# Kernel tuning notes

Measured on AMD Instinct MI355X. Metric: run time of the kernel, lower is better.

Reference implementation:

```python
import jax, jax.numpy as jnp
import numpy as np

B, N, DIM, H, DH = 4, 1024, 1024, 16, 64
SCALE = DH ** -0.5

def setup_inputs() -> dict:
    key = jax.random.key(0)
    ks = jax.random.split(key, 6)
    s = DIM ** -0.5
    return {
        "x": jax.random.normal(ks[0], (B, N, DIM), jnp.float32),
        "Wq": jax.random.normal(ks[1], (DIM, H * DH), jnp.float32) * s,
        "Wk": jax.random.normal(ks[2], (DIM, H * DH), jnp.float32) * s,
        "Wv": jax.random.normal(ks[3], (DIM, H * DH), jnp.float32) * s,
        "Wo": jax.random.normal(ks[4], (H * DH, DIM), jnp.float32) * s,
        "bo": jnp.zeros((DIM,), jnp.float32),
    }

def reference(x, Wq, Wk, Wv, Wo, bo):
    # context is None -> context = x (self-attention), no mask
    split = lambda t: t.reshape(B, N, H, DH).transpose(0, 2, 1, 3)  # b n (h d) -> b h n d
    q = split(x @ Wq)
    k = split(x @ Wk)
    v = split(x @ Wv)
    dots = jnp.einsum('bhid,bhjd->bhij', q, k) * SCALE
    attn = jax.nn.softmax(dots, axis=-1)
    out = jnp.einsum('bhij,bhjd->bhid', attn, v)
    out = out.transpose(0, 2, 1, 3).reshape(B, N, H * DH)  # b h n d -> b n (h d)
    out = out @ Wo + bo  # dropout p=0.0 is identity
    return (out, attn)
```

## Files before the change

### kernel.cpp

```cpp
#include <hip/hip_runtime.h>


#define NN   1024
#define HH   16
#define DHD  64
#define HDD  1024
#define SCALE_ 0.125f

typedef unsigned short ushort_t;
typedef __attribute__((ext_vector_type(8))) short short8;
typedef __attribute__((ext_vector_type(4))) float f32x4;

__device__ __forceinline__ ushort_t f2bf(float f) {
    unsigned int u = __float_as_uint(f);
    u += 0x7fffu + ((u >> 16) & 1u);
    return (ushort_t)(u >> 16);
}

__global__ void transposeW(const float* __restrict__ src, ushort_t* __restrict__ dst) {
    __shared__ ushort_t t[32][33];
    const int bx = blockIdx.x * 32, by = blockIdx.y * 32;
    const int x = threadIdx.x;
#pragma unroll
    for (int yo = 0; yo < 32; yo += 8) {
        int y = threadIdx.y + yo;
        t[y][x] = f2bf(src[(size_t)(by + y) * 1024 + bx + x]);
    }
    __syncthreads();
#pragma unroll
    for (int yo = 0; yo < 32; yo += 8) {
        int y = threadIdx.y + yo;
        dst[(size_t)(bx + y) * 1024 + by + x] = t[x][y];
    }
}

__global__ __launch_bounds__(256)
void gemm_qkv(const float* __restrict__ A,
              const ushort_t* __restrict__ BT0, const ushort_t* __restrict__ BT1,
              const ushort_t* __restrict__ BT2,
              ushort_t* __restrict__ C0, ushort_t* __restrict__ C1,
              ushort_t* __restrict__ C2) {
    __shared__ __align__(16) ushort_t As[128][72];
    __shared__ __align__(16) ushort_t Bs[128][72];

    const int z = blockIdx.z;
    const ushort_t* BT = (z == 0) ? BT0 : (z == 1) ? BT1 : BT2;
    ushort_t* C = (z == 0) ? C0 : (z == 1) ? C1 : C2;
    const int vt_mode = (z == 2) ? 1 : 0;

    const int tid = threadIdx.x;
    const int wave = tid >> 6, lane = tid & 63;
    const int quad = lane >> 4, lr = lane & 15;
    const int wr = (wave >> 1) << 6;
    const int wc = (wave & 1) << 6;
    const int m0 = blockIdx.y << 7;
    const int n0 = blockIdx.x << 7;

    f32x4 acc[4][4];
#pragma unroll
    for (int i = 0; i < 4; i++)
#pragma unroll
        for (int j = 0; j < 4; j++) acc[i][j] = (f32x4){0.f, 0.f, 0.f, 0.f};

    for (int k0 = 0; k0 < 1024; k0 += 64) {
        __syncthreads();
#pragma unroll
        for (int it = 0; it < 4; it++) {
            int idx = tid + it * 256;
            int row = idx >> 3, ch = (idx & 7) << 3;
            const float* ap = A + (size_t)(m0 + row) * 1024 + k0 + ch;
            float4 f0 = *(const float4*)ap;
            float4 f1 = *(const float4*)(ap + 4);
            ushort_t* d = &As[row][ch];
            d[0] = f2bf(f0.x); d[1] = f2bf(f0.y); d[2] = f2bf(f0.z); d[3] = f2bf(f0.w);
            d[4] = f2bf(f1.x); d[5] = f2bf(f1.y); d[6] = f2bf(f1.z); d[7] = f2bf(f1.w);
            *(uint4*)&Bs[row][ch] = *(const uint4*)(BT + (size_t)(n0 + row) * 1024 + k0 + ch);
        }
        __syncthreads();
#pragma unroll
        for (int kk = 0; kk < 64; kk += 32) {
            short8 a[4], b[4];
#pragma unroll
            for (int i = 0; i < 4; i++)
                a[i] = *(const short8*)&As[wr + i * 16 + lr][kk + quad * 8];
#pragma unroll
            for (int j = 0; j < 4; j++)
                b[j] = *(const short8*)&Bs[wc + j * 16 + lr][kk + quad * 8];
#pragma unroll
            for (int i = 0; i < 4; i++)
#pragma unroll
                for (int j = 0; j < 4; j++)
                    acc[i][j] = __builtin_amdgcn_mfma_f32_16x16x32_bf16(
                        a[i], b[j], acc[i][j], 0, 0, 0);
        }
    }

    if (vt_mode == 0) {
#pragma unroll
        for (int i = 0; i < 4; i++)
#pragma unroll
            for (int j = 0; j < 4; j++) {
                int col = n0 + wc + j * 16 + lr;
                int rowb = m0 + wr + i * 16 + quad * 4;
#pragma unroll
                for (int ii = 0; ii < 4; ii++)
                    C[(size_t)(rowb + ii) * 1024 + col] = f2bf(acc[i][j][ii]);
            }
    } else {
#pragma unroll
        for (int i = 0; i < 4; i++)
#pragma unroll
            for (int j = 0; j < 4; j++) {
                int c = n0 + wc + j * 16 + lr;
                int h = c >> 6, d = c & 63;
                int rowb = m0 + wr + i * 16 + quad * 4;
#pragma unroll
                for (int ii = 0; ii < 4; ii++) {
                    int m = rowb + ii;
                    int b_ = m >> 10, n_ = m & 1023;
                    C[((size_t)((b_ * HH + h) * DHD + d) << 10) + n_] = f2bf(acc[i][j][ii]);
                }
            }
    }
}

__global__ __launch_bounds__(256)
void gemm_out(const ushort_t* __restrict__ A, const ushort_t* __restrict__ BT,
              const float* __restrict__ bias, float* __restrict__ C) {
    __shared__ __align__(16) ushort_t As[128][72];
    __shared__ __align__(16) ushort_t Bs[128][72];

    const int tid = threadIdx.x;
    const int wave = tid >> 6, lane = tid & 63;
    const int quad = lane >> 4, lr = lane & 15;
    const int wr = (wave >> 1) << 6;
    const int wc = (wave & 1) << 6;
    const int m0 = blockIdx.y << 7;
    const int n0 = blockIdx.x << 7;

    f32x4 acc[4][4];
#pragma unroll
    for (int i = 0; i < 4; i++)
#pragma unroll
        for (int j = 0; j < 4; j++) acc[i][j] = (f32x4){0.f, 0.f, 0.f, 0.f};

    for (int k0 = 0; k0 < 1024; k0 += 64) {
        __syncthreads();
#pragma unroll
        for (int it = 0; it < 4; it++) {
            int idx = tid + it * 256;
            int row = idx >> 3, ch = (idx & 7) << 3;
            *(uint4*)&As[row][ch] = *(const uint4*)(A + (size_t)(m0 + row) * 1024 + k0 + ch);
            *(uint4*)&Bs[row][ch] = *(const uint4*)(BT + (size_t)(n0 + row) * 1024 + k0 + ch);
        }
        __syncthreads();
#pragma unroll
        for (int kk = 0; kk < 64; kk += 32) {
            short8 a[4], b[4];
#pragma unroll
            for (int i = 0; i < 4; i++)
                a[i] = *(const short8*)&As[wr + i * 16 + lr][kk + quad * 8];
#pragma unroll
            for (int j = 0; j < 4; j++)
                b[j] = *(const short8*)&Bs[wc + j * 16 + lr][kk + quad * 8];
#pragma unroll
            for (int i = 0; i < 4; i++)
#pragma unroll
                for (int j = 0; j < 4; j++)
                    acc[i][j] = __builtin_amdgcn_mfma_f32_16x16x32_bf16(
                        a[i], b[j], acc[i][j], 0, 0, 0);
        }
    }

#pragma unroll
    for (int i = 0; i < 4; i++)
#pragma unroll
        for (int j = 0; j < 4; j++) {
            int col = n0 + wc + j * 16 + lr;
            float badd = bias[col];
            int rowb = m0 + wr + i * 16 + quad * 4;
#pragma unroll
            for (int ii = 0; ii < 4; ii++)
                C[(size_t)(rowb + ii) * 1024 + col] = acc[i][j][ii] + badd;
        }
}

__global__ __launch_bounds__(256)
void attn_kernel(const ushort_t* __restrict__ Q, const ushort_t* __restrict__ K,
                 const ushort_t* __restrict__ VT, float* __restrict__ attn,
                 ushort_t* __restrict__ O) {
    __shared__ __align__(16) ushort_t Qs[64][72];
    __shared__ __align__(16) ushort_t Ks[128][72];
    __shared__ __align__(16) ushort_t Vs[64][136];
    __shared__ __align__(16) ushort_t Ps[64][136];

    const int tid = threadIdx.x;
    const int wave = tid >> 6, lane = tid & 63;
    const int quad = lane >> 4, lr = lane & 15;
    const int q0 = blockIdx.x << 6;
    const int h = blockIdx.y;
    const int b = blockIdx.z;

    const ushort_t* Qb = Q + (size_t)b * NN * HDD + h * DHD;
    const ushort_t* Kb = K + (size_t)b * NN * HDD + h * DHD;
    const ushort_t* VTb = VT + (size_t)(b * HH + h) * DHD * NN;
    float* attn_b = attn + (size_t)(b * HH + h) * NN * NN;
    ushort_t* Ob = O + (size_t)b * NN * HDD + h * DHD;

#pragma unroll
    for (int it = 0; it < 2; it++) {
        int idx = tid + it * 256;
        int row = idx >> 3, ch = (idx & 7) << 3;
        *(uint4*)&Qs[row][ch] = *(const uint4*)(Qb + (size_t)(q0 + row) * HDD + ch);
    }
    __syncthreads();
    const short8 aq0 = *(const short8*)&Qs[wave * 16 + lr][quad * 8];
    const short8 aq1 = *(const short8*)&Qs[wave * 16 + lr][32 + quad * 8];

    float m_i[4], l_i[4];
#pragma unroll
    for (int ii = 0; ii < 4; ii++) { m_i[ii] = -1e30f; l_i[ii] = 0.f; }

    for (int kb = 0; kb < 8; kb++) {
        __syncthreads();
#pragma unroll
        for (int it = 0; it < 4; it++) {
            int idx = tid + it * 256;
            int row = idx >> 3, ch = (idx & 7) << 3;
            *(uint4*)&Ks[row][ch] =
                *(const uint4*)(Kb + (size_t)(kb * 128 + row) * HDD + ch);
        }
        __syncthreads();
        f32x4 s[8];
#pragma unroll
        for (int cb = 0; cb < 8; cb++) {
            s[cb] = (f32x4){0.f, 0.f, 0.f, 0.f};
            short8 b0 = *(const short8*)&Ks[cb * 16 + lr][quad * 8];
            short8 b1 = *(const short8*)&Ks[cb * 16 + lr][32 + quad * 8];
            s[cb] = __builtin_amdgcn_mfma_f32_16x16x32_bf16(aq0, b0, s[cb], 0, 0, 0);
            s[cb] = __builtin_amdgcn_mfma_f32_16x16x32_bf16(aq1, b1, s[cb], 0, 0, 0);
        }
#pragma unroll
        for (int ii = 0; ii < 4; ii++) {
            float rmax = -1e30f;
#pragma unroll
            for (int cb = 0; cb < 8; cb++) rmax = fmaxf(rmax, s[cb][ii]);
            rmax *= SCALE_;
#pragma unroll
            for (int off = 1; off < 16; off <<= 1)
                rmax = fmaxf(rmax, __shfl_xor(rmax, off));
            float mnew = fmaxf(m_i[ii], rmax);
            float psum = 0.f;
#pragma unroll
            for (int cb = 0; cb < 8; cb++) psum += __expf(s[cb][ii] * SCALE_ - mnew);
#pragma unroll
            for (int off = 1; off < 16; off <<= 1) psum += __shfl_xor(psum, off);
            l_i[ii] = l_i[ii] * __expf(m_i[ii] - mnew) + psum;
            m_i[ii] = mnew;
        }
    }
    float inv_l[4];
#pragma unroll
    for (int ii = 0; ii < 4; ii++) inv_l[ii] = 1.f / l_i[ii];

    f32x4 oacc[4];
#pragma unroll
    for (int db = 0; db < 4; db++) oacc[db] = (f32x4){0.f, 0.f, 0.f, 0.f};

    for (int kb = 0; kb < 8; kb++) {
        __syncthreads();
#pragma unroll
        for (int it = 0; it < 8; it++) {
            int idx = tid + it * 256;
            if (idx < 1024) {
                int row = idx >> 3, ch = (idx & 7) << 3;
                *(uint4*)&Ks[row][ch] =
                    *(const uint4*)(Kb + (size_t)(kb * 128 + row) * HDD + ch);
            } else {
                int j = idx - 1024;
                int row = j >> 4, ch = (j & 15) << 3;
                *(uint4*)&Vs[row][ch] =
                    *(const uint4*)(VTb + (size_t)row * NN + kb * 128 + ch);
            }
        }
        __syncthreads();
        f32x4 s[8];
#pragma unroll
        for (int cb = 0; cb < 8; cb++) {
            s[cb] = (f32x4){0.f, 0.f, 0.f, 0.f};
            short8 b0 = *(const short8*)&Ks[cb * 16 + lr][quad * 8];
            short8 b1 = *(const short8*)&Ks[cb * 16 + lr][32 + quad * 8];
            s[cb] = __builtin_amdgcn_mfma_f32_16x16x32_bf16(aq0, b0, s[cb], 0, 0, 0);
            s[cb] = __builtin_amdgcn_mfma_f32_16x16x32_bf16(aq1, b1, s[cb], 0, 0, 0);
        }
#pragma unroll
        for (int cb = 0; cb < 8; cb++)
#pragma unroll
            for (int ii = 0; ii < 4; ii++) {
                float p = __expf(s[cb][ii] * SCALE_ - m_i[ii]) * inv_l[ii];
                Ps[wave * 16 + quad * 4 + ii][cb * 16 + lr] = f2bf(p);
                attn_b[(size_t)(q0 + wave * 16 + quad * 4 + ii) * NN +
                       kb * 128 + cb * 16 + lr] = p;
            }
        __syncthreads();
#pragma unroll
        for (int ks = 0; ks < 4; ks++) {
            short8 ap = *(const short8*)&Ps[wave * 16 + lr][ks * 32 + quad * 8];
#pragma unroll
            for (int db = 0; db < 4; db++) {
                short8 bv = *(const short8*)&Vs[db * 16 + lr][ks * 32 + quad * 8];
                oacc[db] = __builtin_amdgcn_mfma_f32_16x16x32_bf16(ap, bv, oacc[db], 0, 0, 0);
            }
        }
    }
#pragma unroll
    for (int db = 0; db < 4; db++)
#pragma unroll
        for (int ii = 0; ii < 4; ii++) {
            int row = q0 + wave * 16 + quad * 4 + ii;
            Ob[(size_t)row * HDD + db * 16 + lr] = f2bf(oacc[db][ii]);
        }
}

extern "C" void kernel_launch(void* const* d_in, const int* in_sizes, int n_in,
                              void* d_out, int out_size, void* d_ws, size_t ws_size,
                              hipStream_t stream) {
    const float* x  = (const float*)d_in[0];
    const float* Wq = (const float*)d_in[1];
    const float* Wk = (const float*)d_in[2];
    const float* Wv = (const float*)d_in[3];
    const float* Wo = (const float*)d_in[4];
    const float* bo = (const float*)d_in[5];

    float* out  = (float*)d_out;
    float* attn = out + (size_t)4 * 1024 * 1024;

    ushort_t* ws  = (ushort_t*)d_ws;
    ushort_t* WqT = ws;
    ushort_t* WkT = ws + (size_t)1 * 1048576;
    ushort_t* WvT = ws + (size_t)2 * 1048576;
    ushort_t* WoT = ws + (size_t)3 * 1048576;
    ushort_t* Qw  = ws + (size_t)4 * 1048576;
    ushort_t* Kw  = ws + (size_t)8 * 1048576;
    ushort_t* VTw = ws + (size_t)12 * 1048576;
    ushort_t* Ow  = ws + (size_t)16 * 1048576;

    dim3 tb(32, 8), tg(32, 32);
    transposeW<<<tg, tb, 0, stream>>>(Wq, WqT);
    transposeW<<<tg, tb, 0, stream>>>(Wk, WkT);
    transposeW<<<tg, tb, 0, stream>>>(Wv, WvT);
    transposeW<<<tg, tb, 0, stream>>>(Wo, WoT);

    gemm_qkv<<<dim3(8, 32, 3), 256, 0, stream>>>(x, WqT, WkT, WvT, Qw, Kw, VTw);

    attn_kernel<<<dim3(16, 16, 4), 256, 0, stream>>>(Qw, Kw, VTw, attn, Ow);

    gemm_out<<<dim3(8, 32), 256, 0, stream>>>(Ow, WoT, bo, out);
}
```

Baseline: 469.0 us.

## Make attention single-pass by dropping max-subtraction and deferring normalization

The attention kernel no longer runs a separate pass to find the row max and softmax denominator. Instead it computes exp(s*scale) directly, accumulates the row sums and the unnormalized P·V in one pass, and normalizes the output at the end. The bf16 probabilities are kept in registers so the attention matrix can be written after normalization. This removes the duplicate K load and QK^T MFMA pass, at the cost of overflow risk for large logits, bf16-rounded attention values and higher register use. Separately, x is converted to bf16 once up front, the four weight transposes are merged into one launch, and the attention kernel gets a min-blocks launch bound.

```diff
diff --git a/kernel.cpp b/kernel.cpp
--- a/kernel.cpp
+++ b/kernel.cpp
@@ -16,9 +16,28 @@
     u += 0x7fffu + ((u >> 16) & 1u);
     return (ushort_t)(u >> 16);
 }
-
-__global__ void transposeW(const float* __restrict__ src, ushort_t* __restrict__ dst) {
+__device__ __forceinline__ float bfbits2f(unsigned int bits16) {
+    return __uint_as_float(bits16 << 16);
+}
+
+__global__ void convert_x(const float* __restrict__ src, ushort_t* __restrict__ dst) {
+    int i = (blockIdx.x * 256 + threadIdx.x) * 8;
+    float4 f0 = *(const float4*)(src + i);
+    float4 f1 = *(const float4*)(src + i + 4);
+    unsigned int u0 = (unsigned)f2bf(f0.x) | ((unsigned)f2bf(f0.y) << 16);
+    unsigned int u1 = (unsigned)f2bf(f0.z) | ((unsigned)f2bf(f0.w) << 16);
+    unsigned int u2 = (unsigned)f2bf(f1.x) | ((unsigned)f2bf(f1.y) << 16);
+    unsigned int u3 = (unsigned)f2bf(f1.z) | ((unsigned)f2bf(f1.w) << 16);
+    *(uint4*)(dst + i) = (uint4){u0, u1, u2, u3};
+}
+
+__global__ void transposeW4(const float* __restrict__ W0, const float* __restrict__ W1,
+                            const float* __restrict__ W2, const float* __restrict__ W3,
+                            ushort_t* __restrict__ dstBase) {
     __shared__ ushort_t t[32][33];
+    const int z = blockIdx.z;
+    const float* src = (z == 0) ? W0 : (z == 1) ? W1 : (z == 2) ? W2 : W3;
+    ushort_t* dst = dstBase + ((size_t)z << 20);
     const int bx = blockIdx.x * 32, by = blockIdx.y * 32;
     const int x = threadIdx.x;
 #pragma unroll
@@ -35,16 +54,15 @@
 }
 
 __global__ __launch_bounds__(256)
-void gemm_qkv(const float* __restrict__ A,
-              const ushort_t* __restrict__ BT0, const ushort_t* __restrict__ BT1,
-              const ushort_t* __restrict__ BT2,
+void gemm_qkv(const ushort_t* __restrict__ A,
+              const ushort_t* __restrict__ BTbase,
               ushort_t* __restrict__ C0, ushort_t* __restrict__ C1,
               ushort_t* __restrict__ C2) {
     __shared__ __align__(16) ushort_t As[128][72];
     __shared__ __align__(16) ushort_t Bs[128][72];
 
     const int z = blockIdx.z;
-    const ushort_t* BT = (z == 0) ? BT0 : (z == 1) ? BT1 : BT2;
+    const ushort_t* BT = BTbase + ((size_t)z << 20);
     ushort_t* C = (z == 0) ? C0 : (z == 1) ? C1 : C2;
     const int vt_mode = (z == 2) ? 1 : 0;
 
@@ -68,12 +86,7 @@
         for (int it = 0; it < 4; it++) {
             int idx = tid + it * 256;
             int row = idx >> 3, ch = (idx & 7) << 3;
-            const float* ap = A + (size_t)(m0 + row) * 1024 + k0 + ch;
-            float4 f0 = *(const float4*)ap;
-            float4 f1 = *(const float4*)(ap + 4);
-            ushort_t* d = &As[row][ch];
-            d[0] = f2bf(f0.x); d[1] = f2bf(f0.y); d[2] = f2bf(f0.z); d[3] = f2bf(f0.w);
-            d[4] = f2bf(f1.x); d[5] = f2bf(f1.y); d[6] = f2bf(f1.z); d[7] = f2bf(f1.w);
+            *(uint4*)&As[row][ch] = *(const uint4*)(A + (size_t)(m0 + row) * 1024 + k0 + ch);
             *(uint4*)&Bs[row][ch] = *(const uint4*)(BT + (size_t)(n0 + row) * 1024 + k0 + ch);
         }
         __syncthreads();
@@ -185,7 +198,7 @@
         }
 }
 
-__global__ __launch_bounds__(256)
+__global__ __launch_bounds__(256, 2)
 void attn_kernel(const ushort_t* __restrict__ Q, const ushort_t* __restrict__ K,
                  const ushort_t* __restrict__ VT, float* __restrict__ attn,
                  ushort_t* __restrict__ O) {
@@ -217,56 +230,13 @@
     const short8 aq0 = *(const short8*)&Qs[wave * 16 + lr][quad * 8];
     const short8 aq1 = *(const short8*)&Qs[wave * 16 + lr][32 + quad * 8];
 
-    float m_i[4], l_i[4];
-#pragma unroll
-    for (int ii = 0; ii < 4; ii++) { m_i[ii] = -1e30f; l_i[ii] = 0.f; }
-
-    for (int kb = 0; kb < 8; kb++) {
-        __syncthreads();
-#pragma unroll
-        for (int it = 0; it < 4; it++) {
-            int idx = tid + it * 256;
-            int row = idx >> 3, ch = (idx & 7) << 3;
-            *(uint4*)&Ks[row][ch] =
-                *(const uint4*)(Kb + (size_t)(kb * 128 + row) * HDD + ch);
-        }
-        __syncthreads();
-        f32x4 s[8];
-#pragma unroll
-        for (int cb = 0; cb < 8; cb++) {
-            s[cb] = (f32x4){0.f, 0.f, 0.f, 0.f};
-            short8 b0 = *(const short8*)&Ks[cb * 16 + lr][quad * 8];
-            short8 b1 = *(const short8*)&Ks[cb * 16 + lr][32 + quad * 8];
-            s[cb] = __builtin_amdgcn_mfma_f32_16x16x32_bf16(aq0, b0, s[cb], 0, 0, 0);
-            s[cb] = __builtin_amdgcn_mfma_f32_16x16x32_bf16(aq1, b1, s[cb], 0, 0, 0);
-        }
-#pragma unroll
-        for (int ii = 0; ii < 4; ii++) {
-            float rmax = -1e30f;
-#pragma unroll
-            for (int cb = 0; cb < 8; cb++) rmax = fmaxf(rmax, s[cb][ii]);
-            rmax *= SCALE_;
-#pragma unroll
-            for (int off = 1; off < 16; off <<= 1)
-                rmax = fmaxf(rmax, __shfl_xor(rmax, off));
-            float mnew = fmaxf(m_i[ii], rmax);
-            float psum = 0.f;
-#pragma unroll
-            for (int cb = 0; cb < 8; cb++) psum += __expf(s[cb][ii] * SCALE_ - mnew);
-#pragma unroll
-            for (int off = 1; off < 16; off <<= 1) psum += __shfl_xor(psum, off);
-            l_i[ii] = l_i[ii] * __expf(m_i[ii] - mnew) + psum;
-            m_i[ii] = mnew;
-        }
-    }
-    float inv_l[4];
-#pragma unroll
-    for (int ii = 0; ii < 4; ii++) inv_l[ii] = 1.f / l_i[ii];
-
+    unsigned int Pst[8][16];
+    float psum[4] = {0.f, 0.f, 0.f, 0.f};
     f32x4 oacc[4];
 #pragma unroll
     for (int db = 0; db < 4; db++) oacc[db] = (f32x4){0.f, 0.f, 0.f, 0.f};
 
+#pragma unroll
     for (int kb = 0; kb < 8; kb++) {
         __syncthreads();
 #pragma unroll
@@ -284,6 +254,7 @@
             }
         }
         __syncthreads();
+
         f32x4 s[8];
 #pragma unroll
         for (int cb = 0; cb < 8; cb++) {
@@ -293,16 +264,21 @@
             s[cb] = __builtin_amdgcn_mfma_f32_16x16x32_bf16(aq0, b0, s[cb], 0, 0, 0);
             s[cb] = __builtin_amdgcn_mfma_f32_16x16x32_bf16(aq1, b1, s[cb], 0, 0, 0);
         }
-#pragma unroll
-        for (int cb = 0; cb < 8; cb++)
+
+#pragma unroll
+        for (int cb = 0; cb < 8; cb++) {
+            ushort_t pb[4];
 #pragma unroll
             for (int ii = 0; ii < 4; ii++) {
-                float p = __expf(s[cb][ii] * SCALE_ - m_i[ii]) * inv_l[ii];
-                Ps[wave * 16 + quad * 4 + ii][cb * 16 + lr] = f2bf(p);
-                attn_b[(size_t)(q0 + wave * 16 + quad * 4 + ii) * NN +
-                       kb * 128 + cb * 16 + lr] = p;
-            }
-        __syncthreads();
+                float p = __expf(s[cb][ii] * SCALE_);
+                psum[ii] += p;
+                pb[ii] = f2bf(p);
+                Ps[wave * 16 + quad * 4 + ii][cb * 16 + lr] = pb[ii];
+            }
+            Pst[kb][cb * 2]     = (unsigned)pb[0] | ((unsigned)pb[1] << 16);
+            Pst[kb][cb * 2 + 1] = (unsigned)pb[2] | ((unsigned)pb[3] << 16);
+        }
+
 #pragma unroll
         for (int ks = 0; ks < 4; ks++) {
             short8 ap = *(const short8*)&Ps[wave * 16 + lr][ks * 32 + quad * 8];
@@ -313,12 +289,39 @@
             }
         }
     }
+
+    float inv_l[4];
+#pragma unroll
+    for (int ii = 0; ii < 4; ii++) {
+        float v = psum[ii];
+#pragma unroll
+        for (int off = 1; off < 16; off <<= 1) v += __shfl_xor(v, off);
+        inv_l[ii] = 1.f / v;
+    }
+
 #pragma unroll
     for (int db = 0; db < 4; db++)
 #pragma unroll
         for (int ii = 0; ii < 4; ii++) {
             int row = q0 + wave * 16 + quad * 4 + ii;
-            Ob[(size_t)row * HDD + db * 16 + lr] = f2bf(oacc[db][ii]);
+            Ob[(size_t)row * HDD + db * 16 + lr] = f2bf(oacc[db][ii] * inv_l[ii]);
+        }
+
+#pragma unroll
+    for (int kb = 0; kb < 8; kb++)
+#pragma unroll
+        for (int cb = 0; cb < 8; cb++) {
+            unsigned int lo = Pst[kb][cb * 2];
+            unsigned int hi = Pst[kb][cb * 2 + 1];
+            float p0 = bfbits2f(lo & 0xffffu) * inv_l[0];
+            float p1 = bfbits2f(lo >> 16)     * inv_l[1];
+            float p2 = bfbits2f(hi & 0xffffu) * inv_l[2];
+            float p3 = bfbits2f(hi >> 16)     * inv_l[3];
+            size_t base = (size_t)(q0 + wave * 16 + quad * 4) * NN + kb * 128 + cb * 16 + lr;
+            attn_b[base]          = p0;
+            attn_b[base + NN]     = p1;
+            attn_b[base + 2 * NN] = p2;
+            attn_b[base + 3 * NN] = p3;
         }
 }
 
@@ -336,24 +339,19 @@
     float* attn = out + (size_t)4 * 1024 * 1024;
 
     ushort_t* ws  = (ushort_t*)d_ws;
-    ushort_t* WqT = ws;
-    ushort_t* WkT = ws + (size_t)1 * 1048576;
-    ushort_t* WvT = ws + (size_t)2 * 1048576;
-    ushort_t* WoT = ws + (size_t)3 * 1048576;
-    ushort_t* Qw  = ws + (size_t)4 * 1048576;
-    ushort_t* Kw  = ws + (size_t)8 * 1048576;
-    ushort_t* VTw = ws + (size_t)12 * 1048576;
-    ushort_t* Ow  = ws + (size_t)16 * 1048576;
-
-    dim3 tb(32, 8), tg(32, 32);
-    transposeW<<<tg, tb, 0, stream>>>(Wq, WqT);
-    transposeW<<<tg, tb, 0, stream>>>(Wk, WkT);
-    transposeW<<<tg, tb, 0, stream>>>(Wv, WvT);
-    transposeW<<<tg, tb, 0, stream>>>(Wo, WoT);
-
-    gemm_qkv<<<dim3(8, 32, 3), 256, 0, stream>>>(x, WqT, WkT, WvT, Qw, Kw, VTw);
+    ushort_t* WT  = ws;
+    ushort_t* xb  = ws + (size_t)4 * 1048576;
+    ushort_t* Qw  = ws + (size_t)8 * 1048576;
+    ushort_t* Kw  = ws + (size_t)12 * 1048576;
+    ushort_t* VTw = ws + (size_t)16 * 1048576;
+    ushort_t* Ow  = ws + (size_t)20 * 1048576;
+
+    convert_x<<<2048, 256, 0, stream>>>(x, xb);
+    transposeW4<<<dim3(32, 32, 4), dim3(32, 8), 0, stream>>>(Wq, Wk, Wv, Wo, WT);
+
+    gemm_qkv<<<dim3(8, 32, 3), 256, 0, stream>>>(xb, WT, Qw, Kw, VTw);
 
     attn_kernel<<<dim3(16, 16, 4), 256, 0, stream>>>(Qw, Kw, VTw, attn, Ow);
 
-    gemm_out<<<dim3(8, 32), 256, 0, stream>>>(Ow, WoT, bo, out);
-}
+    gemm_out<<<dim3(8, 32), 256, 0, stream>>>(Ow, WT + (size_t)3 * 1048576, bo, out);
+}
```

Measured after the change: 638.0 us. +36.0%, slower.
